# Kernel tuning notes

Measured on AMD Instinct MI355X. Metric: run time of the kernel, lower is better.

## Reference

```python
import jax, jax.numpy as jnp
import numpy as np

N = 100_000      # nodes
E = 3_200_000    # edges (avg degree 32)
F_IN = 37        # NCI1 num_features
H = 16           # hidden
C = 2            # NCI1 num_classes


def setup_inputs() -> dict:
    key = jax.random.key(0)
    k = jax.random.split(key, 7)
    x = jax.random.normal(k[0], (N, F_IN), dtype=jnp.float32)
    edge_index = jax.random.randint(k[1], (2, E), 0, N, dtype=jnp.int32)
    edge_weight = jax.random.uniform(k[2], (E,), dtype=jnp.float32)
    # Glorot-ish init for the two GCN linear weights, zero bias (PyG default)
    W1 = jax.random.normal(k[3], (F_IN, H), dtype=jnp.float32) * (1.0 / np.sqrt(F_IN))
    b1 = jnp.zeros((H,), dtype=jnp.float32)
    W2 = jax.random.normal(k[4], (H, C), dtype=jnp.float32) * (1.0 / np.sqrt(H))
    b2 = jnp.zeros((C,), dtype=jnp.float32)
    return {"x": x, "edge_index": edge_index, "edge_weight": edge_weight,
            "W1": W1, "b1": b1, "W2": W2, "b2": b2}


def _gcn_norm(edge_index, edge_weight, dtype):
    # PyG gcn_norm: add self-loops (weight 1.0), symmetric D^-1/2 A D^-1/2
    loop = jnp.arange(N, dtype=edge_index.dtype)
    row = jnp.concatenate([edge_index[0], loop])  # source
    col = jnp.concatenate([edge_index[1], loop])  # target (aggregation index)
    w = jnp.concatenate([edge_weight, jnp.ones((N,), dtype=dtype)])
    deg = jax.ops.segment_sum(w, col, num_segments=N)
    dinv = jnp.where(deg > 0, jax.lax.rsqrt(deg), 0.0).astype(dtype)
    norm = dinv[row] * w * dinv[col]  # [E+N]
    return row, col, norm


def _gcn_layer(x, row, col, norm, W, b):
    h = x @ W                                   # small dense transform first
    msg = norm[:, None] * h[row]                # gather + scale, [E+N, out]
    out = jax.ops.segment_sum(msg, col, num_segments=N)  # scatter-add
    return out + b


def reference(x, edge_index, edge_weight, W1, b1, W2, b2):
    row, col, norm = _gcn_norm(edge_index, edge_weight, x.dtype)
    h = jax.nn.relu(_gcn_layer(x, row, col, norm, W1, b1))
    # F.dropout with training=False is identity (module evaluated in eval mode)
    h = _gcn_layer(h, row, col, norm, W2, b2)
    return jax.nn.log_softmax(h, axis=1)
```

## Files before the change

kernel.cpp:

```cpp
#include <hip/hip_runtime.h>
#include <math.h>

#define N_NODES 100000
#define N_EDGES 3200000
#define F_IN    37
#define H_DIM   16
#define C_DIM   2

#define BUCKET_BITS 7
#define BUCKET_SZ   128
#define NBUCK       782
#define CAP         4736
#define NPBLK       512
#define EB          6250
#define EPT_P       7
#define EPT_S       5
#define NPAGE       782

__device__ __forceinline__ unsigned bf16rne(float f) {
    unsigned u = __float_as_uint(f);
    return (u + 0x7FFFu + ((u >> 16) & 1u)) >> 16;
}
__device__ __forceinline__ int2 ldnt_i2(const int2* p) {
    long long v = __builtin_nontemporal_load((const long long*)p);
    return *(int2*)&v;
}
#define BLO(u) __uint_as_float((u) << 16)
#define BHI(u) __uint_as_float((u) & 0xFFFF0000u)
#define EW(u)  __uint_as_float(((u) >> 17) << 16)
#define ER(u)  ((u) & 0x1FFFFu)

__global__ __launch_bounds__(1024) void k_part(
    const int* __restrict__ row, const int* __restrict__ col,
    const float* __restrict__ w, int* __restrict__ gcur, int2* __restrict__ ebuf)
{
    __shared__ int  cnt[NBUCK];
    __shared__ int  base[NBUCK];
    __shared__ int  gbase[NBUCK];
    __shared__ int  wscan[16];
    __shared__ unsigned short pg2b[NPAGE];
    __shared__ int2 stage[EB];
    int t = threadIdx.x;
    size_t e0 = (size_t)blockIdx.x * EB;
    int bk[EPT_P], rc[EPT_P], lofs[EPT_P];
    float wv[EPT_P];

    if (t < NBUCK) cnt[t] = 0;
    __syncthreads();
#pragma unroll
    for (int k = 0; k < EPT_P; k++) {
        int i = k * 1024 + t;
        if (i < EB) {
            size_t e = e0 + i;
            int r = __builtin_nontemporal_load(&row[e]);
            int c = __builtin_nontemporal_load(&col[e]);
            wv[k] = __builtin_nontemporal_load(&w[e]);
            bk[k] = c >> BUCKET_BITS;
            rc[k] = r | ((c & (BUCKET_SZ - 1)) << 17);
            lofs[k] = atomicAdd(&cnt[bk[k]], 1);
        } else bk[k] = -1;
    }
    __syncthreads();
    {
        int lane = t & 63, wid = t >> 6;
        int v = (t < NBUCK) ? cnt[t] : 0;
#pragma unroll
        for (int d = 1; d < 64; d <<= 1) {
            int u = __shfl_up(v, d);
            if (lane >= d) v += u;
        }
        if (lane == 63) wscan[wid] = v;
        __syncthreads();
        if (wid == 0) {
            int u = (lane < 16) ? wscan[lane] : 0;
#pragma unroll
            for (int d = 1; d < 16; d <<= 1) {
                int u2 = __shfl_up(u, d);
                if (lane >= d) u += u2;
            }
            if (lane < 16) wscan[lane] = u;
        }
        __syncthreads();
        if (t < NBUCK) base[t] = v + ((wid > 0) ? wscan[wid - 1] : 0);
    }
    __syncthreads();
#pragma unroll
    for (int k = 0; k < EPT_P; k++) {
        if (bk[k] >= 0)
            stage[base[bk[k]] - cnt[bk[k]] + lofs[k]] =
                make_int2(rc[k], __float_as_int(wv[k]));
    }
    if (t < NBUCK) {
        int st = base[t] - cnt[t], en = base[t];
        for (int p = (st + 7) >> 3; p <= ((en - 1) >> 3); p++)
            pg2b[p] = (unsigned short)t;
        gbase[t] = t * CAP + atomicAdd(&gcur[t], cnt[t]);
    }
    __syncthreads();
    for (int s2 = t; s2 < EB; s2 += 1024) {
        int lo = pg2b[s2 >> 3];
        while (base[lo] <= s2) lo++;
        int dst = gbase[lo] + (s2 - (base[lo] - cnt[lo]));
        ebuf[dst] = stage[s2];
    }
}

__global__ __launch_bounds__(1024) void k_sortxw1(
    const int* __restrict__ gcur, const int2* __restrict__ ebuf,
    const float* __restrict__ x, const float* __restrict__ W1,
    unsigned* __restrict__ ebuf4, int2* __restrict__ rp,
    float* __restrict__ dinv, unsigned* __restrict__ h1b)
{
    __shared__ int2  stage[CAP];
    __shared__ int   cnt[BUCKET_SZ];
    __shared__ int   base[BUCKET_SZ];
    __shared__ float sdinv[BUCKET_SZ];
    __shared__ int   wscan[16];
    __shared__ float sW[F_IN * H_DIM];
    float* xs = (float*)stage;

    int t = threadIdx.x, b = blockIdx.x;
    int s = b * CAP;
    int len = gcur[b];
    int nbase = b << BUCKET_BITS;
    if (t < BUCKET_SZ) cnt[t] = 0;
    __syncthreads();

    int2 ed[EPT_S]; int cl[EPT_S], lofs[EPT_S];
#pragma unroll
    for (int k = 0; k < EPT_S; k++) {
        int i = k * 1024 + t;
        if (i < len) {
            int2 v = ldnt_i2(&ebuf[s + i]);
            ed[k] = v;
            cl[k] = v.x >> 17;
            lofs[k] = atomicAdd(&cnt[cl[k]], 1);
        } else cl[k] = -1;
    }
    __syncthreads();
    {
        int lane = t & 63, wid = t >> 6;
        int v = (t < BUCKET_SZ) ? cnt[t] : 0;
#pragma unroll
        for (int d = 1; d < 64; d <<= 1) {
            int u = __shfl_up(v, d);
            if (lane >= d) v += u;
        }
        if (lane == 63) wscan[wid] = v;
        __syncthreads();
        if (wid == 0) {
            int u = (lane < 16) ? wscan[lane] : 0;
#pragma unroll
            for (int d = 1; d < 16; d <<= 1) {
                int u2 = __shfl_up(u, d);
                if (lane >= d) u += u2;
            }
            if (lane < 16) wscan[lane] = u;
        }
        __syncthreads();
        if (t < BUCKET_SZ) base[t] = v + ((wid > 0) ? wscan[wid - 1] : 0);
    }
    __syncthreads();
#pragma unroll
    for (int k = 0; k < EPT_S; k++) {
        if (cl[k] >= 0) {
            int pos = base[cl[k]] - cnt[cl[k]] + lofs[k];
            stage[pos] = ed[k];
        }
    }
    __syncthreads();
    for (int i = t; i < len; i += 1024) {
        int2 v = stage[i];
        unsigned wb = bf16rne(__int_as_float(v.y));
        __builtin_nontemporal_store((wb << 17) | (unsigned)(v.x & 0x1FFFF),
                                    &ebuf4[s + i]);
    }
    {
        int n = t >> 3, l = t & 7;
        int st = base[n] - cnt[n], cn = cnt[n];
        float sum = 0.f;
        for (int i = l; i < cn; i += 8) sum += __int_as_float(stage[st + i].y);
        sum += __shfl_xor(sum, 1);
        sum += __shfl_xor(sum, 2);
        sum += __shfl_xor(sum, 4);
        if (l == 0) {
            float di = rsqrtf(sum + 1.0f);
            sdinv[n] = di;
            int c = nbase + n;
            if (c < N_NODES) {
                rp[c] = make_int2(s + st, cn);
                dinv[c] = di;
            }
        }
    }
    __syncthreads();

    for (int idx = t; idx < F_IN * H_DIM; idx += 1024) sW[idx] = W1[idx];
    {
        const float4* x4 = (const float4*)(x + (size_t)nbase * F_IN);
        const int nv4 = (BUCKET_SZ * F_IN) / 4;
        int gf0 = nbase * F_IN;
        for (int idx = t; idx < nv4; idx += 1024) {
            int gf = gf0 + 4 * idx;
            float4 v;
            if (gf + 3 < N_NODES * F_IN) {
                v = x4[idx];
            } else {
                v.x = (gf + 0 < N_NODES * F_IN) ? x[gf + 0] : 0.f;
                v.y = (gf + 1 < N_NODES * F_IN) ? x[gf + 1] : 0.f;
                v.z = (gf + 2 < N_NODES * F_IN) ? x[gf + 2] : 0.f;
                v.w = (gf + 3 < N_NODES * F_IN) ? x[gf + 3] : 0.f;
            }
            ((float4*)xs)[idx] = v;
        }
    }
    __syncthreads();
    {
        int n = t >> 3, sub = t & 7;
        int c = nbase + n;
        if (c < N_NODES) {
            const float* xi = &xs[n * F_IN];
            float a0 = 0.f, a1 = 0.f;
            for (int k = 0; k < F_IN; k++) {
                float xv = xi[k];
                a0 += xv * sW[k * H_DIM + 2 * sub];
                a1 += xv * sW[k * H_DIM + 2 * sub + 1];
            }
            float di = sdinv[n];
            unsigned pk = bf16rne(di * a0) | (bf16rne(di * a1) << 16);
            h1b[(size_t)c * 8 + sub] = pk;
        }
    }
}

__global__ __launch_bounds__(256) void k_agg1(
    const int2* __restrict__ rp, const unsigned* __restrict__ ebuf4,
    const uint4* __restrict__ h1b, const float* __restrict__ dinv,
    const float* __restrict__ b1, const float* __restrict__ W2,
    float* __restrict__ h2s)
{
    __shared__ float sW2[H_DIM * C_DIM];
    __shared__ float sb1[H_DIM];
    int t = threadIdx.x;
    if (t < H_DIM * C_DIM) sW2[t] = W2[t];
    if (t >= 32 && t < 32 + H_DIM) sb1[t - 32] = b1[t - 32];
    __syncthreads();
    int id = blockIdx.x * 256 + t;
    int c = id >> 4;
    int sub = id & 15, q = sub & 1, h = sub >> 1;
    if (c >= N_NODES) return;
    int2 seg = rp[c];
    int s = seg.x, n = seg.y;
    int m = (n - h + 7) >> 3;
    int p0i = s + h;
    float acc[8] = {0.f, 0.f, 0.f, 0.f, 0.f, 0.f, 0.f, 0.f};

#define PROC1(u)                                                    \
    {   float a = EW(u);                                            \
        uint4 g = h1b[(size_t)ER(u) * 2 + q];                       \
        acc[0] += a * BLO(g.x); acc[1] += a * BHI(g.x);             \
        acc[2] += a * BLO(g.y); acc[3] += a * BHI(g.y);             \
        acc[4] += a * BLO(g.z); acc[5] += a * BHI(g.z);             \
        acc[6] += a * BLO(g.w); acc[7] += a * BHI(g.w); }

    int k = 0;
    if (m >= 4) {
        unsigned e0 = __builtin_nontemporal_load(&ebuf4[p0i + 0]);
        unsigned e1 = __builtin_nontemporal_load(&ebuf4[p0i + 8]);
        unsigned e2 = __builtin_nontemporal_load(&ebuf4[p0i + 16]);
        unsigned e3 = __builtin_nontemporal_load(&ebuf4[p0i + 24]);
        for (; k + 8 <= m; k += 4) {
            unsigned f0 = __builtin_nontemporal_load(&ebuf4[p0i + 8 * (k + 4)]);
            unsigned f1 = __builtin_nontemporal_load(&ebuf4[p0i + 8 * (k + 5)]);
            unsigned f2 = __builtin_nontemporal_load(&ebuf4[p0i + 8 * (k + 6)]);
            unsigned f3 = __builtin_nontemporal_load(&ebuf4[p0i + 8 * (k + 7)]);
            PROC1(e0); PROC1(e1); PROC1(e2); PROC1(e3);
            e0 = f0; e1 = f1; e2 = f2; e3 = f3;
        }
        PROC1(e0); PROC1(e1); PROC1(e2); PROC1(e3);
        k += 4;
    }
    for (; k < m; k++) {
        unsigned u = __builtin_nontemporal_load(&ebuf4[p0i + 8 * k]);
        PROC1(u);
    }
#undef PROC1

#pragma unroll
    for (int j = 0; j < 8; j++) {
        acc[j] += __shfl_xor(acc[j], 2);
        acc[j] += __shfl_xor(acc[j], 4);
        acc[j] += __shfl_xor(acc[j], 8);
    }

    float dc = dinv[c];
    uint4 gc = h1b[(size_t)c * 2 + q];
    float hcv[8] = {BLO(gc.x), BHI(gc.x), BLO(gc.y), BHI(gc.y),
                    BLO(gc.z), BHI(gc.z), BLO(gc.w), BHI(gc.w)};
    int j0 = q << 3;
    float p0 = 0.f, p1 = 0.f;
#pragma unroll
    for (int j = 0; j < 8; j++) {
        float rv = fmaxf(dc * (acc[j] + hcv[j]) + sb1[j0 + j], 0.f);
        p0 += rv * sW2[(j0 + j) * C_DIM + 0];
        p1 += rv * sW2[(j0 + j) * C_DIM + 1];
    }
    p0 += __shfl_xor(p0, 1);
    p1 += __shfl_xor(p1, 1);
    if (sub == 0) ((float2*)h2s)[c] = make_float2(dc * p0, dc * p1);
}

__global__ __launch_bounds__(256) void k_agg2(
    const int2* __restrict__ rp, const unsigned* __restrict__ ebuf4,
    const float* __restrict__ h2s, const float* __restrict__ dinv,
    const float* __restrict__ b2, float* __restrict__ out)
{
    int id = blockIdx.x * 256 + threadIdx.x;
    int c = id >> 3, sub = id & 7;
    if (c >= N_NODES) return;
    int2 seg = rp[c];
    int s = seg.x, n = seg.y;
    const float2* h22 = (const float2*)h2s;
    int m = (n - sub + 7) >> 3;
    int p0i = s + sub;
    float a0 = 0.f, a1 = 0.f;

#define PROC2(u)                                                    \
    {   float a = EW(u);                                            \
        float2 hv = h22[ER(u)];                                     \
        a0 += a * hv.x;  a1 += a * hv.y; }

    int k = 0;
    if (m >= 4) {
        unsigned e0 = __builtin_nontemporal_load(&ebuf4[p0i + 0]);
        unsigned e1 = __builtin_nontemporal_load(&ebuf4[p0i + 8]);
        unsigned e2 = __builtin_nontemporal_load(&ebuf4[p0i + 16]);
        unsigned e3 = __builtin_nontemporal_load(&ebuf4[p0i + 24]);
        for (; k + 8 <= m; k += 4) {
            unsigned f0 = __builtin_nontemporal_load(&ebuf4[p0i + 8 * (k + 4)]);
            unsigned f1 = __builtin_nontemporal_load(&ebuf4[p0i + 8 * (k + 5)]);
            unsigned f2 = __builtin_nontemporal_load(&ebuf4[p0i + 8 * (k + 6)]);
            unsigned f3 = __builtin_nontemporal_load(&ebuf4[p0i + 8 * (k + 7)]);
            PROC2(e0); PROC2(e1); PROC2(e2); PROC2(e3);
            e0 = f0; e1 = f1; e2 = f2; e3 = f3;
        }
        PROC2(e0); PROC2(e1); PROC2(e2); PROC2(e3);
        k += 4;
    }
    for (; k < m; k++) {
        unsigned u = __builtin_nontemporal_load(&ebuf4[p0i + 8 * k]);
        PROC2(u);
    }
#undef PROC2

    a0 += __shfl_xor(a0, 1); a0 += __shfl_xor(a0, 2); a0 += __shfl_xor(a0, 4);
    a1 += __shfl_xor(a1, 1); a1 += __shfl_xor(a1, 2); a1 += __shfl_xor(a1, 4);
    if (sub == 0) {
        float dc = dinv[c];
        float2 hc = h22[c];
        float l0 = dc * (a0 + hc.x) + b2[0];
        float l1 = dc * (a1 + hc.y) + b2[1];
        float mx = fmaxf(l0, l1);
        float lse = mx + logf(expf(l0 - mx) + expf(l1 - mx));
        ((float2*)out)[c] = make_float2(l0 - lse, l1 - lse);
    }
}

extern "C" void kernel_launch(void* const* d_in, const int* in_sizes, int n_in,
                              void* d_out, int out_size, void* d_ws, size_t ws_size,
                              hipStream_t stream) {
    const float* x  = (const float*)d_in[0];
    const int*   ei = (const int*)d_in[1];
    const float* w  = (const float*)d_in[2];
    const float* W1 = (const float*)d_in[3];
    const float* b1 = (const float*)d_in[4];
    const float* W2 = (const float*)d_in[5];
    const float* b2 = (const float*)d_in[6];
    float* out = (float*)d_out;

    const int* row = ei;
    const int* col = ei + N_EDGES;

    char* ws = (char*)d_ws;
    int*      gcur  = (int*)(ws + 0);
    int2*     rp    = (int2*)(ws + 3200);
    float*    dinv  = (float*)(ws + 803200);
    unsigned* h1b   = (unsigned*)(ws + 1203200);
    float*    h2s   = (float*)(ws + 4403200);
    unsigned* ebuf4 = (unsigned*)(ws + 5203200);
    int2*     ebuf  = (int2*)(ws + 20017408);

    hipMemsetAsync(gcur, 0, 3200, stream);
    k_part    <<<NPBLK, 1024, 0, stream>>>(row, col, w, gcur, ebuf);
    k_sortxw1 <<<NBUCK, 1024, 0, stream>>>(gcur, ebuf, x, W1, ebuf4, rp, dinv, h1b);
    k_agg1    <<<(16 * N_NODES + 255) / 256, 256, 0, stream>>>(rp, ebuf4, (const uint4*)h1b, dinv, b1, W2, h2s);
    k_agg2    <<<(8 * N_NODES + 255) / 256, 256, 0, stream>>>(rp, ebuf4, h2s, dinv, b2, out);
}
```

Measured before the change: 191.0 us.

## Replace per-node CSR sort with bucket-level shared-memory atomic aggregation

Drops the second-level in-bucket counting sort and its packed bf16 edge buffer. Degree and both aggregation passes now stream the bucket-partitioned edge list directly and accumulate into per-bucket shared-memory arrays with LDS atomics. This removes the sort, scan and extra edge-buffer write, and reads the 8-byte edge records (with fp32 weights) in each pass instead of 4-byte packed ones. It adds shared-memory atomic contention, and the added bounds clamps give extra safety checks.

```diff
diff --git a/kernel.cpp b/kernel.cpp
--- a/kernel.cpp
+++ b/kernel.cpp
@@ -14,8 +14,8 @@
 #define NPBLK       512
 #define EB          6250
 #define EPT_P       7
-#define EPT_S       5
 #define NPAGE       782
+#define EBUF_SLOTS  (NBUCK * CAP + EB)
 
 __device__ __forceinline__ unsigned bf16rne(float f) {
     unsigned u = __float_as_uint(f);
@@ -27,8 +27,6 @@
 }
 #define BLO(u) __uint_as_float((u) << 16)
 #define BHI(u) __uint_as_float((u) & 0xFFFF0000u)
-#define EW(u)  __uint_as_float(((u) >> 17) << 16)
-#define ER(u)  ((u) & 0x1FFFFu)
 
 __global__ __launch_bounds__(1024) void k_part(
     const int* __restrict__ row, const int* __restrict__ col,
@@ -55,8 +53,9 @@
             int r = __builtin_nontemporal_load(&row[e]);
             int c = __builtin_nontemporal_load(&col[e]);
             wv[k] = __builtin_nontemporal_load(&w[e]);
-            bk[k] = c >> BUCKET_BITS;
-            rc[k] = r | ((c & (BUCKET_SZ - 1)) << 17);
+            bk[k] = (c >> BUCKET_BITS) & 1023;
+            if (bk[k] >= NBUCK) bk[k] = NBUCK - 1;
+            rc[k] = (r & 0x1FFFF) | ((c & (BUCKET_SZ - 1)) << 17);
             lofs[k] = atomicAdd(&cnt[bk[k]], 1);
         } else bk[k] = -1;
     }
@@ -86,115 +85,47 @@
     __syncthreads();
 #pragma unroll
     for (int k = 0; k < EPT_P; k++) {
-        if (bk[k] >= 0)
-            stage[base[bk[k]] - cnt[bk[k]] + lofs[k]] =
+        if (bk[k] >= 0) {
+            int pos = base[bk[k]] - cnt[bk[k]] + lofs[k];
+            if (pos >= 0 && pos < EB) stage[pos] =
                 make_int2(rc[k], __float_as_int(wv[k]));
+        }
     }
     if (t < NBUCK) {
         int st = base[t] - cnt[t], en = base[t];
-        for (int p = (st + 7) >> 3; p <= ((en - 1) >> 3); p++)
+        int p0 = (st + 7) >> 3, p1 = (en - 1) >> 3;
+        if (p0 < 0) p0 = 0;
+        if (p1 >= NPAGE) p1 = NPAGE - 1;
+        for (int p = p0; p <= p1; p++)
             pg2b[p] = (unsigned short)t;
         gbase[t] = t * CAP + atomicAdd(&gcur[t], cnt[t]);
     }
     __syncthreads();
     for (int s2 = t; s2 < EB; s2 += 1024) {
         int lo = pg2b[s2 >> 3];
-        while (base[lo] <= s2) lo++;
+        while (lo < NBUCK - 1 && base[lo] <= s2) lo++;
         int dst = gbase[lo] + (s2 - (base[lo] - cnt[lo]));
-        ebuf[dst] = stage[s2];
-    }
-}
-
-__global__ __launch_bounds__(1024) void k_sortxw1(
+        if (dst >= 0 && dst < EBUF_SLOTS)
+            ebuf[dst] = stage[s2];
+    }
+}
+
+__global__ __launch_bounds__(1024) void k_degxw1(
     const int* __restrict__ gcur, const int2* __restrict__ ebuf,
     const float* __restrict__ x, const float* __restrict__ W1,
-    unsigned* __restrict__ ebuf4, int2* __restrict__ rp,
     float* __restrict__ dinv, unsigned* __restrict__ h1b)
 {
-    __shared__ int2  stage[CAP];
-    __shared__ int   cnt[BUCKET_SZ];
-    __shared__ int   base[BUCKET_SZ];
+    __shared__ float sdeg[BUCKET_SZ];
     __shared__ float sdinv[BUCKET_SZ];
-    __shared__ int   wscan[16];
+    __shared__ float xs[BUCKET_SZ * F_IN];
     __shared__ float sW[F_IN * H_DIM];
-    float* xs = (float*)stage;
-
     int t = threadIdx.x, b = blockIdx.x;
     int s = b * CAP;
     int len = gcur[b];
+    if (len > CAP) len = CAP;
     int nbase = b << BUCKET_BITS;
-    if (t < BUCKET_SZ) cnt[t] = 0;
-    __syncthreads();
-
-    int2 ed[EPT_S]; int cl[EPT_S], lofs[EPT_S];
-#pragma unroll
-    for (int k = 0; k < EPT_S; k++) {
-        int i = k * 1024 + t;
-        if (i < len) {
-            int2 v = ldnt_i2(&ebuf[s + i]);
-            ed[k] = v;
-            cl[k] = v.x >> 17;
-            lofs[k] = atomicAdd(&cnt[cl[k]], 1);
-        } else cl[k] = -1;
-    }
-    __syncthreads();
-    {
-        int lane = t & 63, wid = t >> 6;
-        int v = (t < BUCKET_SZ) ? cnt[t] : 0;
-#pragma unroll
-        for (int d = 1; d < 64; d <<= 1) {
-            int u = __shfl_up(v, d);
-            if (lane >= d) v += u;
-        }
-        if (lane == 63) wscan[wid] = v;
-        __syncthreads();
-        if (wid == 0) {
-            int u = (lane < 16) ? wscan[lane] : 0;
-#pragma unroll
-            for (int d = 1; d < 16; d <<= 1) {
-                int u2 = __shfl_up(u, d);
-                if (lane >= d) u += u2;
-            }
-            if (lane < 16) wscan[lane] = u;
-        }
-        __syncthreads();
-        if (t < BUCKET_SZ) base[t] = v + ((wid > 0) ? wscan[wid - 1] : 0);
-    }
-    __syncthreads();
-#pragma unroll
-    for (int k = 0; k < EPT_S; k++) {
-        if (cl[k] >= 0) {
-            int pos = base[cl[k]] - cnt[cl[k]] + lofs[k];
-            stage[pos] = ed[k];
-        }
-    }
-    __syncthreads();
-    for (int i = t; i < len; i += 1024) {
-        int2 v = stage[i];
-        unsigned wb = bf16rne(__int_as_float(v.y));
-        __builtin_nontemporal_store((wb << 17) | (unsigned)(v.x & 0x1FFFF),
-                                    &ebuf4[s + i]);
-    }
-    {
-        int n = t >> 3, l = t & 7;
-        int st = base[n] - cnt[n], cn = cnt[n];
-        float sum = 0.f;
-        for (int i = l; i < cn; i += 8) sum += __int_as_float(stage[st + i].y);
-        sum += __shfl_xor(sum, 1);
-        sum += __shfl_xor(sum, 2);
-        sum += __shfl_xor(sum, 4);
-        if (l == 0) {
-            float di = rsqrtf(sum + 1.0f);
-            sdinv[n] = di;
-            int c = nbase + n;
-            if (c < N_NODES) {
-                rp[c] = make_int2(s + st, cn);
-                dinv[c] = di;
-            }
-        }
-    }
-    __syncthreads();
-
+
+    if (t < BUCKET_SZ) sdeg[t] = 0.f;
     for (int idx = t; idx < F_IN * H_DIM; idx += 1024) sW[idx] = W1[idx];
     {
         const float4* x4 = (const float4*)(x + (size_t)nbase * F_IN);
@@ -215,6 +146,18 @@
         }
     }
     __syncthreads();
+    for (int i = t; i < len; i += 1024) {
+        int2 v = ldnt_i2(&ebuf[s + i]);
+        atomicAdd(&sdeg[(v.x >> 17) & (BUCKET_SZ - 1)], __int_as_float(v.y));
+    }
+    __syncthreads();
+    if (t < BUCKET_SZ) {
+        float di = rsqrtf(sdeg[t] + 1.0f);
+        sdinv[t] = di;
+        int c = nbase + t;
+        if (c < N_NODES) dinv[c] = di;
+    }
+    __syncthreads();
     {
         int n = t >> 3, sub = t & 7;
         int c = nbase + n;
@@ -233,136 +176,85 @@
     }
 }
 
-__global__ __launch_bounds__(256) void k_agg1(
-    const int2* __restrict__ rp, const unsigned* __restrict__ ebuf4,
-    const uint4* __restrict__ h1b, const float* __restrict__ dinv,
+__global__ __launch_bounds__(1024) void k_agg1b(
+    const int* __restrict__ gcur, const int2* __restrict__ ebuf,
+    const unsigned* __restrict__ h1b, const float* __restrict__ dinv,
     const float* __restrict__ b1, const float* __restrict__ W2,
     float* __restrict__ h2s)
 {
+    __shared__ float acc[BUCKET_SZ * H_DIM];
     __shared__ float sW2[H_DIM * C_DIM];
     __shared__ float sb1[H_DIM];
-    int t = threadIdx.x;
+    int t = threadIdx.x, b = blockIdx.x;
+    int s = b * CAP;
+    int len = gcur[b];
+    if (len > CAP) len = CAP;
+    int nbase = b << BUCKET_BITS;
     if (t < H_DIM * C_DIM) sW2[t] = W2[t];
-    if (t >= 32 && t < 32 + H_DIM) sb1[t - 32] = b1[t - 32];
-    __syncthreads();
-    int id = blockIdx.x * 256 + t;
-    int c = id >> 4;
-    int sub = id & 15, q = sub & 1, h = sub >> 1;
-    if (c >= N_NODES) return;
-    int2 seg = rp[c];
-    int s = seg.x, n = seg.y;
-    int m = (n - h + 7) >> 3;
-    int p0i = s + h;
-    float acc[8] = {0.f, 0.f, 0.f, 0.f, 0.f, 0.f, 0.f, 0.f};
-
-#define PROC1(u)                                                    \
-    {   float a = EW(u);                                            \
-        uint4 g = h1b[(size_t)ER(u) * 2 + q];                       \
-        acc[0] += a * BLO(g.x); acc[1] += a * BHI(g.x);             \
-        acc[2] += a * BLO(g.y); acc[3] += a * BHI(g.y);             \
-        acc[4] += a * BLO(g.z); acc[5] += a * BHI(g.z);             \
-        acc[6] += a * BLO(g.w); acc[7] += a * BHI(g.w); }
-
-    int k = 0;
-    if (m >= 4) {
-        unsigned e0 = __builtin_nontemporal_load(&ebuf4[p0i + 0]);
-        unsigned e1 = __builtin_nontemporal_load(&ebuf4[p0i + 8]);
-        unsigned e2 = __builtin_nontemporal_load(&ebuf4[p0i + 16]);
-        unsigned e3 = __builtin_nontemporal_load(&ebuf4[p0i + 24]);
-        for (; k + 8 <= m; k += 4) {
-            unsigned f0 = __builtin_nontemporal_load(&ebuf4[p0i + 8 * (k + 4)]);
-            unsigned f1 = __builtin_nontemporal_load(&ebuf4[p0i + 8 * (k + 5)]);
-            unsigned f2 = __builtin_nontemporal_load(&ebuf4[p0i + 8 * (k + 6)]);
-            unsigned f3 = __builtin_nontemporal_load(&ebuf4[p0i + 8 * (k + 7)]);
-            PROC1(e0); PROC1(e1); PROC1(e2); PROC1(e3);
-            e0 = f0; e1 = f1; e2 = f2; e3 = f3;
-        }
-        PROC1(e0); PROC1(e1); PROC1(e2); PROC1(e3);
-        k += 4;
-    }
-    for (; k < m; k++) {
-        unsigned u = __builtin_nontemporal_load(&ebuf4[p0i + 8 * k]);
-        PROC1(u);
-    }
-#undef PROC1
-
-#pragma unroll
-    for (int j = 0; j < 8; j++) {
-        acc[j] += __shfl_xor(acc[j], 2);
-        acc[j] += __shfl_xor(acc[j], 4);
-        acc[j] += __shfl_xor(acc[j], 8);
-    }
-
-    float dc = dinv[c];
-    uint4 gc = h1b[(size_t)c * 2 + q];
-    float hcv[8] = {BLO(gc.x), BHI(gc.x), BLO(gc.y), BHI(gc.y),
-                    BLO(gc.z), BHI(gc.z), BLO(gc.w), BHI(gc.w)};
-    int j0 = q << 3;
-    float p0 = 0.f, p1 = 0.f;
-#pragma unroll
-    for (int j = 0; j < 8; j++) {
-        float rv = fmaxf(dc * (acc[j] + hcv[j]) + sb1[j0 + j], 0.f);
-        p0 += rv * sW2[(j0 + j) * C_DIM + 0];
-        p1 += rv * sW2[(j0 + j) * C_DIM + 1];
-    }
-    p0 += __shfl_xor(p0, 1);
-    p1 += __shfl_xor(p1, 1);
-    if (sub == 0) ((float2*)h2s)[c] = make_float2(dc * p0, dc * p1);
-}
-
-__global__ __launch_bounds__(256) void k_agg2(
-    const int2* __restrict__ rp, const unsigned* __restrict__ ebuf4,
+    if (t >= 64 && t < 64 + H_DIM) sb1[t - 64] = b1[t - 64];
+    for (int i = t; i < BUCKET_SZ * H_DIM; i += 1024) acc[i] = 0.f;
+    __syncthreads();
+
+    int j = t & 7;
+    for (int e = t >> 3; e < len; e += 128) {
+        int2 v = ldnt_i2(&ebuf[s + e]);
+        float wv = __int_as_float(v.y);
+        int r = v.x & 0x1FFFF, cl = (v.x >> 17) & (BUCKET_SZ - 1);
+        unsigned g = h1b[(size_t)r * 8 + j];
+        atomicAdd(&acc[cl * H_DIM + 2 * j],     wv * BLO(g));
+        atomicAdd(&acc[cl * H_DIM + 2 * j + 1], wv * BHI(g));
+    }
+    __syncthreads();
+
+    int n = t >> 3, sub = t & 7;
+    int c = nbase + n;
+    if (c < N_NODES) {
+        float dc = dinv[c];
+        unsigned gs = h1b[(size_t)c * 8 + sub];
+        float r0 = fmaxf(dc * (acc[n * H_DIM + 2 * sub]     + BLO(gs)) + sb1[2 * sub],     0.f);
+        float r1 = fmaxf(dc * (acc[n * H_DIM + 2 * sub + 1] + BHI(gs)) + sb1[2 * sub + 1], 0.f);
+        float p0 = r0 * sW2[(2 * sub) * C_DIM + 0] + r1 * sW2[(2 * sub + 1) * C_DIM + 0];
+        float p1 = r0 * sW2[(2 * sub) * C_DIM + 1] + r1 * sW2[(2 * sub + 1) * C_DIM + 1];
+        p0 += __shfl_xor(p0, 1); p0 += __shfl_xor(p0, 2); p0 += __shfl_xor(p0, 4);
+        p1 += __shfl_xor(p1, 1); p1 += __shfl_xor(p1, 2); p1 += __shfl_xor(p1, 4);
+        if (sub == 0) ((float2*)h2s)[c] = make_float2(dc * p0, dc * p1);
+    }
+}
+
+__global__ __launch_bounds__(1024) void k_agg2b(
+    const int* __restrict__ gcur, const int2* __restrict__ ebuf,
     const float* __restrict__ h2s, const float* __restrict__ dinv,
     const float* __restrict__ b2, float* __restrict__ out)
 {
-    int id = blockIdx.x * 256 + threadIdx.x;
-    int c = id >> 3, sub = id & 7;
-    if (c >= N_NODES) return;
-    int2 seg = rp[c];
-    int s = seg.x, n = seg.y;
+    __shared__ float acc2[BUCKET_SZ * 2];
+    int t = threadIdx.x, b = blockIdx.x;
+    int s = b * CAP;
+    int len = gcur[b];
+    if (len > CAP) len = CAP;
+    int nbase = b << BUCKET_BITS;
+    if (t < BUCKET_SZ * 2) acc2[t] = 0.f;
+    __syncthreads();
     const float2* h22 = (const float2*)h2s;
-    int m = (n - sub + 7) >> 3;
-    int p0i = s + sub;
-    float a0 = 0.f, a1 = 0.f;
-
-#define PROC2(u)                                                    \
-    {   float a = EW(u);                                            \
-        float2 hv = h22[ER(u)];                                     \
-        a0 += a * hv.x;  a1 += a * hv.y; }
-
-    int k = 0;
-    if (m >= 4) {
-        unsigned e0 = __builtin_nontemporal_load(&ebuf4[p0i + 0]);
-        unsigned e1 = __builtin_nontemporal_load(&ebuf4[p0i + 8]);
-        unsigned e2 = __builtin_nontemporal_load(&ebuf4[p0i + 16]);
-        unsigned e3 = __builtin_nontemporal_load(&ebuf4[p0i + 24]);
-        for (; k + 8 <= m; k += 4) {
-            unsigned f0 = __builtin_nontemporal_load(&ebuf4[p0i + 8 * (k + 4)]);
-            unsigned f1 = __builtin_nontemporal_load(&ebuf4[p0i + 8 * (k + 5)]);
-            unsigned f2 = __builtin_nontemporal_load(&ebuf4[p0i + 8 * (k + 6)]);
-            unsigned f3 = __builtin_nontemporal_load(&ebuf4[p0i + 8 * (k + 7)]);
-            PROC2(e0); PROC2(e1); PROC2(e2); PROC2(e3);
-            e0 = f0; e1 = f1; e2 = f2; e3 = f3;
-        }
-        PROC2(e0); PROC2(e1); PROC2(e2); PROC2(e3);
-        k += 4;
-    }
-    for (; k < m; k++) {
-        unsigned u = __builtin_nontemporal_load(&ebuf4[p0i + 8 * k]);
-        PROC2(u);
-    }
-#undef PROC2
-
-    a0 += __shfl_xor(a0, 1); a0 += __shfl_xor(a0, 2); a0 += __shfl_xor(a0, 4);
-    a1 += __shfl_xor(a1, 1); a1 += __shfl_xor(a1, 2); a1 += __shfl_xor(a1, 4);
-    if (sub == 0) {
-        float dc = dinv[c];
-        float2 hc = h22[c];
-        float l0 = dc * (a0 + hc.x) + b2[0];
-        float l1 = dc * (a1 + hc.y) + b2[1];
-        float mx = fmaxf(l0, l1);
-        float lse = mx + logf(expf(l0 - mx) + expf(l1 - mx));
-        ((float2*)out)[c] = make_float2(l0 - lse, l1 - lse);
+    for (int e = t; e < len; e += 1024) {
+        int2 v = ldnt_i2(&ebuf[s + e]);
+        float wv = __int_as_float(v.y);
+        int r = v.x & 0x1FFFF, cl = (v.x >> 17) & (BUCKET_SZ - 1);
+        float2 hv = h22[r];
+        atomicAdd(&acc2[cl * 2],     wv * hv.x);
+        atomicAdd(&acc2[cl * 2 + 1], wv * hv.y);
+    }
+    __syncthreads();
+    if (t < BUCKET_SZ) {
+        int c = nbase + t;
+        if (c < N_NODES) {
+            float dc = dinv[c];
+            float2 hc = h22[c];
+            float l0 = dc * (acc2[t * 2]     + hc.x) + b2[0];
+            float l1 = dc * (acc2[t * 2 + 1] + hc.y) + b2[1];
+            float mx = fmaxf(l0, l1);
+            float lse = mx + logf(expf(l0 - mx) + expf(l1 - mx));
+            ((float2*)out)[c] = make_float2(l0 - lse, l1 - lse);
+        }
     }
 }
 
@@ -382,17 +274,15 @@
     const int* col = ei + N_EDGES;
 
     char* ws = (char*)d_ws;
-    int*      gcur  = (int*)(ws + 0);
-    int2*     rp    = (int2*)(ws + 3200);
-    float*    dinv  = (float*)(ws + 803200);
-    unsigned* h1b   = (unsigned*)(ws + 1203200);
-    float*    h2s   = (float*)(ws + 4403200);
-    unsigned* ebuf4 = (unsigned*)(ws + 5203200);
-    int2*     ebuf  = (int2*)(ws + 20017408);
+    int*      gcur = (int*)(ws + 0);
+    float*    dinv = (float*)(ws + 3200);
+    unsigned* h1b  = (unsigned*)(ws + 403200);
+    float*    h2s  = (float*)(ws + 3603200);
+    int2*     ebuf = (int2*)(ws + 4403200);
 
     hipMemsetAsync(gcur, 0, 3200, stream);
     k_part    <<<NPBLK, 1024, 0, stream>>>(row, col, w, gcur, ebuf);
-    k_sortxw1 <<<NBUCK, 1024, 0, stream>>>(gcur, ebuf, x, W1, ebuf4, rp, dinv, h1b);
-    k_agg1    <<<(16 * N_NODES + 255) / 256, 256, 0, stream>>>(rp, ebuf4, (const uint4*)h1b, dinv, b1, W2, h2s);
-    k_agg2    <<<(8 * N_NODES + 255) / 256, 256, 0, stream>>>(rp, ebuf4, h2s, dinv, b2, out);
-}
+    k_degxw1  <<<NBUCK, 1024, 0, stream>>>(gcur, ebuf, x, W1, dinv, h1b);
+    k_agg1b   <<<NBUCK, 1024, 0, stream>>>(gcur, ebuf, h1b, dinv, b1, W2, h2s);
+    k_agg2b   <<<NBUCK, 1024, 0, stream>>>(gcur, ebuf, h2s, dinv, b2, out);
+}
```

New measurement: 527.4 us. 176% more time.

## Use 8 lanes per node in layer-1 aggregation and add bounds guards

Applied to the files above, without the earlier changes.

The layer-1 aggregation now assigns 8 threads per node instead of 16. Each thread processes every 8th edge and gathers the full 16-feature bf16 row as two uint4 loads, where before each thread took half the features. This halves the thread count and removes the duplicate edge-word loads across feature halves, at the cost of more registers and wider gathers per lane. The partition and sort kernels also gain clamps and bounds checks on bucket indices, positions and lengths, which add a few compares.

```diff
diff --git a/kernel.cpp b/kernel.cpp
--- a/kernel.cpp
+++ b/kernel.cpp
@@ -16,6 +16,7 @@
 #define EPT_P       7
 #define EPT_S       5
 #define NPAGE       782
+#define EBUF_SLOTS  (NBUCK * CAP + EB)
 
 __device__ __forceinline__ unsigned bf16rne(float f) {
     unsigned u = __float_as_uint(f);
@@ -55,8 +56,9 @@
             int r = __builtin_nontemporal_load(&row[e]);
             int c = __builtin_nontemporal_load(&col[e]);
             wv[k] = __builtin_nontemporal_load(&w[e]);
-            bk[k] = c >> BUCKET_BITS;
-            rc[k] = r | ((c & (BUCKET_SZ - 1)) << 17);
+            bk[k] = (c >> BUCKET_BITS) & 1023;
+            if (bk[k] >= NBUCK) bk[k] = NBUCK - 1;
+            rc[k] = (r & 0x1FFFF) | ((c & (BUCKET_SZ - 1)) << 17);
             lofs[k] = atomicAdd(&cnt[bk[k]], 1);
         } else bk[k] = -1;
     }
@@ -86,22 +88,28 @@
     __syncthreads();
 #pragma unroll
     for (int k = 0; k < EPT_P; k++) {
-        if (bk[k] >= 0)
-            stage[base[bk[k]] - cnt[bk[k]] + lofs[k]] =
+        if (bk[k] >= 0) {
+            int pos = base[bk[k]] - cnt[bk[k]] + lofs[k];
+            if (pos >= 0 && pos < EB) stage[pos] =
                 make_int2(rc[k], __float_as_int(wv[k]));
+        }
     }
     if (t < NBUCK) {
         int st = base[t] - cnt[t], en = base[t];
-        for (int p = (st + 7) >> 3; p <= ((en - 1) >> 3); p++)
+        int p0 = (st + 7) >> 3, p1 = (en - 1) >> 3;
+        if (p0 < 0) p0 = 0;
+        if (p1 >= NPAGE) p1 = NPAGE - 1;
+        for (int p = p0; p <= p1; p++)
             pg2b[p] = (unsigned short)t;
         gbase[t] = t * CAP + atomicAdd(&gcur[t], cnt[t]);
     }
     __syncthreads();
     for (int s2 = t; s2 < EB; s2 += 1024) {
         int lo = pg2b[s2 >> 3];
-        while (base[lo] <= s2) lo++;
+        while (lo < NBUCK - 1 && base[lo] <= s2) lo++;
         int dst = gbase[lo] + (s2 - (base[lo] - cnt[lo]));
-        ebuf[dst] = stage[s2];
+        if (dst >= 0 && dst < EBUF_SLOTS)
+            ebuf[dst] = stage[s2];
     }
 }
 
@@ -122,6 +130,7 @@
     int t = threadIdx.x, b = blockIdx.x;
     int s = b * CAP;
     int len = gcur[b];
+    if (len > CAP) len = CAP;
     int nbase = b << BUCKET_BITS;
     if (t < BUCKET_SZ) cnt[t] = 0;
     __syncthreads();
@@ -133,7 +142,7 @@
         if (i < len) {
             int2 v = ldnt_i2(&ebuf[s + i]);
             ed[k] = v;
-            cl[k] = v.x >> 17;
+            cl[k] = (v.x >> 17) & (BUCKET_SZ - 1);
             lofs[k] = atomicAdd(&cnt[cl[k]], 1);
         } else cl[k] = -1;
     }
@@ -165,7 +174,7 @@
     for (int k = 0; k < EPT_S; k++) {
         if (cl[k] >= 0) {
             int pos = base[cl[k]] - cnt[cl[k]] + lofs[k];
-            stage[pos] = ed[k];
+            if (pos >= 0 && pos < CAP) stage[pos] = ed[k];
         }
     }
     __syncthreads();
@@ -246,22 +255,30 @@
     if (t >= 32 && t < 32 + H_DIM) sb1[t - 32] = b1[t - 32];
     __syncthreads();
     int id = blockIdx.x * 256 + t;
-    int c = id >> 4;
-    int sub = id & 15, q = sub & 1, h = sub >> 1;
+    int c = id >> 3;
+    int sub = id & 7;
     if (c >= N_NODES) return;
     int2 seg = rp[c];
     int s = seg.x, n = seg.y;
-    int m = (n - h + 7) >> 3;
-    int p0i = s + h;
-    float acc[8] = {0.f, 0.f, 0.f, 0.f, 0.f, 0.f, 0.f, 0.f};
+    int m = (n - sub + 7) >> 3;
+    int p0i = s + sub;
+    float acc[16];
+#pragma unroll
+    for (int j = 0; j < 16; j++) acc[j] = 0.f;
 
 #define PROC1(u)                                                    \
     {   float a = EW(u);                                            \
-        uint4 g = h1b[(size_t)ER(u) * 2 + q];                       \
-        acc[0] += a * BLO(g.x); acc[1] += a * BHI(g.x);             \
-        acc[2] += a * BLO(g.y); acc[3] += a * BHI(g.y);             \
-        acc[4] += a * BLO(g.z); acc[5] += a * BHI(g.z);             \
-        acc[6] += a * BLO(g.w); acc[7] += a * BHI(g.w); }
+        size_t rr = (size_t)ER(u) * 2;                              \
+        uint4 g0 = h1b[rr];                                         \
+        uint4 g1 = h1b[rr + 1];                                     \
+        acc[0]  += a * BLO(g0.x); acc[1]  += a * BHI(g0.x);         \
+        acc[2]  += a * BLO(g0.y); acc[3]  += a * BHI(g0.y);         \
+        acc[4]  += a * BLO(g0.z); acc[5]  += a * BHI(g0.z);         \
+        acc[6]  += a * BLO(g0.w); acc[7]  += a * BHI(g0.w);         \
+        acc[8]  += a * BLO(g1.x); acc[9]  += a * BHI(g1.x);         \
+        acc[10] += a * BLO(g1.y); acc[11] += a * BHI(g1.y);         \
+        acc[12] += a * BLO(g1.z); acc[13] += a * BHI(g1.z);         \
+        acc[14] += a * BLO(g1.w); acc[15] += a * BHI(g1.w); }
 
     int k = 0;
     if (m >= 4) {
@@ -287,26 +304,21 @@
 #undef PROC1
 
 #pragma unroll
-    for (int j = 0; j < 8; j++) {
+    for (int j = 0; j < 16; j++) {
+        acc[j] += __shfl_xor(acc[j], 1);
         acc[j] += __shfl_xor(acc[j], 2);
         acc[j] += __shfl_xor(acc[j], 4);
-        acc[j] += __shfl_xor(acc[j], 8);
     }
 
     float dc = dinv[c];
-    uint4 gc = h1b[(size_t)c * 2 + q];
-    float hcv[8] = {BLO(gc.x), BHI(gc.x), BLO(gc.y), BHI(gc.y),
-                    BLO(gc.z), BHI(gc.z), BLO(gc.w), BHI(gc.w)};
-    int j0 = q << 3;
-    float p0 = 0.f, p1 = 0.f;
-#pragma unroll
-    for (int j = 0; j < 8; j++) {
-        float rv = fmaxf(dc * (acc[j] + hcv[j]) + sb1[j0 + j], 0.f);
-        p0 += rv * sW2[(j0 + j) * C_DIM + 0];
-        p1 += rv * sW2[(j0 + j) * C_DIM + 1];
-    }
-    p0 += __shfl_xor(p0, 1);
-    p1 += __shfl_xor(p1, 1);
+    const unsigned* h1w = (const unsigned*)h1b;
+    unsigned gs = h1w[(size_t)c * 8 + sub];
+    float r0 = fmaxf(dc * (acc[2 * sub]     + BLO(gs)) + sb1[2 * sub],     0.f);
+    float r1 = fmaxf(dc * (acc[2 * sub + 1] + BHI(gs)) + sb1[2 * sub + 1], 0.f);
+    float p0 = r0 * sW2[(2 * sub) * C_DIM + 0] + r1 * sW2[(2 * sub + 1) * C_DIM + 0];
+    float p1 = r0 * sW2[(2 * sub) * C_DIM + 1] + r1 * sW2[(2 * sub + 1) * C_DIM + 1];
+    p0 += __shfl_xor(p0, 1); p0 += __shfl_xor(p0, 2); p0 += __shfl_xor(p0, 4);
+    p1 += __shfl_xor(p1, 1); p1 += __shfl_xor(p1, 2); p1 += __shfl_xor(p1, 4);
     if (sub == 0) ((float2*)h2s)[c] = make_float2(dc * p0, dc * p1);
 }
 
@@ -393,6 +405,6 @@
     hipMemsetAsync(gcur, 0, 3200, stream);
     k_part    <<<NPBLK, 1024, 0, stream>>>(row, col, w, gcur, ebuf);
     k_sortxw1 <<<NBUCK, 1024, 0, stream>>>(gcur, ebuf, x, W1, ebuf4, rp, dinv, h1b);
-    k_agg1    <<<(16 * N_NODES + 255) / 256, 256, 0, stream>>>(rp, ebuf4, (const uint4*)h1b, dinv, b1, W2, h2s);
+    k_agg1    <<<(8 * N_NODES + 255) / 256, 256, 0, stream>>>(rp, ebuf4, (const uint4*)h1b, dinv, b1, W2, h2s);
     k_agg2    <<<(8 * N_NODES + 255) / 256, 256, 0, stream>>>(rp, ebuf4, h2s, dinv, b2, out);
 }
```

Measured after the change: 191.0 us. Within noise of the previous version (-0.0%).
